# Kernel tuning notes

Measured on AMD Instinct MI355X. Metric: run time of the kernel, lower is better.

## Reference

```python
import jax, jax.numpy as jnp
import numpy as np

EPS = 1e-9
ALPHA = 1.0
BETA = 6.0
TOPK = 13
NUM_CLASSES = 80


def _make_boxes(key, shape, img=640.0, wh_min=8.0, wh_max=128.0):
    k1, k2 = jax.random.split(key)
    cxy = jax.random.uniform(k1, shape[:-1] + (2,)) * img
    wh = wh_min + jax.random.uniform(k2, shape[:-1] + (2,)) * (wh_max - wh_min)
    return jnp.concatenate([cxy - wh / 2, cxy + wh / 2], axis=-1)


def setup_inputs() -> dict:
    key = jax.random.key(0)
    ks = jax.random.split(key, 5)
    B, N, C, M = 16, 8400, NUM_CLASSES, 64
    pd_scores = jax.random.normal(ks[0], (B, N, C), dtype=jnp.float32)  # logits
    pd_bboxes = _make_boxes(ks[1], (B, N, 4))
    anc_points = jax.random.uniform(ks[2], (N, 2)) * 640.0
    gt_labels = jax.random.randint(ks[3], (B, M, 1), 0, C).astype(jnp.int64)
    gt_bboxes = _make_boxes(ks[4], (B, M, 4), wh_min=16.0, wh_max=256.0)
    mask_gt = jnp.ones((B, M, 1), dtype=jnp.float32)
    return {"pd_scores": pd_scores, "pd_bboxes": pd_bboxes, "anc_points": anc_points,
            "gt_labels": gt_labels, "gt_bboxes": gt_bboxes, "mask_gt": mask_gt}


def _pairwise_iou(gt_bboxes, pd_bboxes):
    # gt: (B,M,4), pd: (B,N,4) -> (B,M,N)
    a1 = gt_bboxes[:, :, None, :2]
    a2 = gt_bboxes[:, :, None, 2:]
    b1 = pd_bboxes[:, None, :, :2]
    b2 = pd_bboxes[:, None, :, 2:]
    inter = jnp.clip(jnp.minimum(a2, b2) - jnp.maximum(a1, b1), 0.0).prod(-1)
    area_a = (a2 - a1).prod(-1)
    area_b = (b2 - b1).prod(-1)
    return inter / jnp.maximum(area_a + area_b - inter, EPS)


def _tal_assign(pd_scores, pd_bboxes, anc_points, gt_labels, gt_bboxes, mask_gt):
    B, N, C = pd_scores.shape
    M = gt_labels.shape[1]
    ps = jax.nn.sigmoid(pd_scores)  # input_is_logits=True
    mask_gt_bool = mask_gt[..., 0] > 0.5  # (B,M)

    # centers-in-boxes mask (B,M,N)
    xy = anc_points[None, None, :, :]
    lt = gt_bboxes[:, :, None, :2]
    rb = gt_bboxes[:, :, None, 2:]
    deltas = jnp.concatenate([xy - lt, rb - xy], axis=-1)  # (B,M,N,4)
    mask_in_gts = deltas.min(-1) > EPS
    valid = mask_in_gts & mask_gt_bool[:, :, None]

    # alignment metric: score(gt class)^alpha * IoU^beta, zero outside valid
    gt_ids = jnp.clip(gt_labels[..., 0], 0)  # (B,M)
    scores_t = jnp.swapaxes(ps, 1, 2)  # (B,C,N)
    bbox_scores = jnp.take_along_axis(scores_t, gt_ids[:, :, None], axis=1)  # (B,M,N)
    ious = _pairwise_iou(gt_bboxes, pd_bboxes)
    ious = jnp.where(valid, ious, 0.0)
    align = jnp.where(valid, (bbox_scores ** ALPHA) * (ious ** BETA), 0.0)

    # top-k anchors per GT along anchor dim
    topv, topi = jax.lax.top_k(align, TOPK)  # (B,M,K)
    sel = (topv > EPS) & mask_gt_bool[:, :, None]
    bi = jnp.arange(B)[:, None, None]
    mi = jnp.arange(M)[None, :, None]
    cnt = jnp.zeros((B, M, N), jnp.int32).at[bi, mi, topi].add(sel.astype(jnp.int32))
    topk_mask = cnt > 0
    mask_pos = (topk_mask & valid).astype(jnp.float32)  # (B,M,N)

    # resolve anchors assigned to multiple GTs: keep highest IoU GT
    fg = mask_pos.sum(axis=1)  # (B,N)
    multi = (fg > 1)[:, None, :]  # (B,1,N)
    best_gt = jnp.argmax(ious, axis=1)  # (B,N)
    is_max = jnp.swapaxes(jax.nn.one_hot(best_gt, M, dtype=mask_pos.dtype), 1, 2)  # (B,M,N)
    mask_pos = jnp.where(multi, is_max, mask_pos)
    fg_mask = mask_pos.sum(axis=1)  # (B,N)
    tgt_gt_idx = jnp.argmax(mask_pos, axis=1)  # (B,N)

    # gather targets
    target_labels = jnp.take_along_axis(gt_labels[..., 0], tgt_gt_idx, axis=1)  # (B,N)
    target_bboxes = jnp.take_along_axis(gt_bboxes, tgt_gt_idx[..., None], axis=1)  # (B,N,4)

    # normalized classification targets
    align = align * mask_pos
    max_align = align.max(axis=1, keepdims=True) + EPS  # (B,1,N)
    per_anchor = (align / max_align * (ious * mask_pos)).sum(axis=1)  # (B,N)
    onehot = jax.nn.one_hot(target_labels, C, dtype=jnp.float32)
    cls_targets = onehot * per_anchor[..., None]  # (B,N,C)
    return target_labels, target_bboxes, cls_targets, fg_mask > 0, tgt_gt_idx


def reference(pd_scores, pd_bboxes, anc_points, gt_labels, gt_bboxes, mask_gt):
    return _tal_assign(pd_scores, pd_bboxes, anc_points, gt_labels, gt_bboxes, mask_gt)
```

## Files before the change

kernel.cpp:

```cpp
#include <hip/hip_runtime.h>
#include <math.h>

#define BB 16
#define NN 8400
#define CC 80
#define MM 64
#define KTOP 13
#define FEPS 1e-9f
#define CAP 2048
#define RPW 8

typedef float floatx4 __attribute__((ext_vector_type(4)));

#define OFF_O1 134400
#define OFF_O2 672000
#define OFF_O3 11424000
#define OFF_O4 11558400
#define CCNT_OFF 9299200
#define CAND_OFF 9300224
#define SCR_OFF  10348800

__device__ __forceinline__ float iou_pair(const float4 g, const float4 p) {
    float ix1 = fmaxf(g.x, p.x);
    float iy1 = fmaxf(g.y, p.y);
    float ix2 = fminf(g.z, p.z);
    float iy2 = fminf(g.w, p.w);
    float iw = fmaxf(ix2 - ix1, 0.0f);
    float ih = fmaxf(iy2 - iy1, 0.0f);
    float inter = iw * ih;
    float aa = (g.z - g.x) * (g.w - g.y);
    float ab = (p.z - p.x) * (p.w - p.y);
    float uni = fmaxf(aa + ab - inter, FEPS);
    return inter / uni;
}

__global__ __launch_bounds__(256) void k_zero2(int* __restrict__ ccnt,
                                               int* __restrict__ scr)
{
    int i = blockIdx.x * 256 + threadIdx.x;
    if (i < 1024) ccnt[i] = 0;
    else if (i < 1024 + 403200) scr[i - 1024] = 0;
}

__global__ __launch_bounds__(256) void k_inbox(
    const float* __restrict__ anc, const float* __restrict__ gt_bboxes,
    const float* __restrict__ mask_gt,
    int* __restrict__ ccnt, unsigned short* __restrict__ cand)
{
    const int b = blockIdx.y;
    const int n = blockIdx.x * 256 + threadIdx.x;
    const int tid = threadIdx.x;

    __shared__ float4 gtb[MM];
    __shared__ int hcnt[MM];
    __shared__ int gbase[MM];

    if (tid < MM) {
        float4 g = *(const float4*)&gt_bboxes[(size_t)(b * MM + tid) * 4];
        if (mask_gt[b * MM + tid] <= 0.5f)
            g = make_float4(1e30f, 1e30f, -1e30f, -1e30f);
        gtb[tid] = g;
        hcnt[tid] = 0;
    }
    __syncthreads();

    float ax = 0.0f, ay = 0.0f;
    const bool inb = n < NN;
    if (inb) { float2 a2 = *(const float2*)&anc[2 * n]; ax = a2.x; ay = a2.y; }

    unsigned long long mask = 0ull;
    #pragma unroll 8
    for (int m = 0; m < MM; ++m) {
        float4 g = gtb[m];
        float d1 = ax - g.x, d2 = ay - g.y, d3 = g.z - ax, d4 = g.w - ay;
        if (inb && fminf(fminf(d1, d2), fminf(d3, d4)) > FEPS)
            mask |= 1ull << m;
    }

    unsigned long long t = mask;
    while (t) { int m = __ffsll(t) - 1; t &= t - 1; atomicAdd(&hcnt[m], 1); }
    __syncthreads();

    if (tid < MM && hcnt[tid] > 0) {
        gbase[tid] = atomicAdd(&ccnt[b * MM + tid], hcnt[tid]);
        hcnt[tid] = 0;
    }
    __syncthreads();

    t = mask;
    while (t) {
        int m = __ffsll(t) - 1; t &= t - 1;
        int slot = gbase[m] + atomicAdd(&hcnt[m], 1);
        if (slot < CAP)
            cand[(size_t)(b * MM + m) * CAP + slot] = (unsigned short)n;
    }
}

__global__ __launch_bounds__(256) void k_topk(
    const float* __restrict__ pd_scores, const float* __restrict__ pd_bboxes,
    const int* __restrict__ gt_labels, const float* __restrict__ gt_bboxes,
    const int* __restrict__ ccnt, const unsigned short* __restrict__ cand,
    int* __restrict__ cntb, int* __restrict__ mselb, float* __restrict__ aselb)
{
    const int bm = blockIdx.x;
    const int b = bm >> 6, m = bm & 63;
    const int tid = threadIdx.x;
    const int lane = tid & 63;
    const int wid = tid >> 6;

    __shared__ unsigned long long cmerge[64];

    const float4 g = *(const float4*)&gt_bboxes[(size_t)bm * 4];
    const int lab  = gt_labels[bm];
    const int labc = lab > 0 ? lab : 0;
    const unsigned epskey = __float_as_uint(FEPS);
    const int count = min(ccnt[bm], CAP);
    const unsigned short* list = cand + (size_t)bm * CAP;
    const float* srow = pd_scores + (size_t)b * NN * CC + labc;
    const float* pbb  = pd_bboxes + (size_t)b * NN * 4;

    unsigned long long e[RPW];
    #pragma unroll
    for (int j = 0; j < RPW; ++j) {
        int i = tid + j * 256;
        unsigned long long v = 0ull;
        if (i < count) {
            int n = list[i];
            float4 p = *(const float4*)&pbb[(size_t)n * 4];
            float io = iou_pair(g, p);
            float x = srow[(size_t)n * CC];
            float s = 1.0f / (1.0f + expf(-x));
            float i2 = io * io;
            unsigned key = __float_as_uint(s * (i2 * i2 * i2));
            v = ((unsigned long long)key << 32) | (unsigned)(NN - n);
        }
        e[j] = v;
    }

    {
        unsigned long long lm = 0ull;
        #pragma unroll
        for (int j = 0; j < RPW; ++j) if (e[j] > lm) lm = e[j];

        unsigned long long winv = 0ull;
        for (int r = 0; r < KTOP; ++r) {
            unsigned long long bv = lm;
            #pragma unroll
            for (int off = 32; off > 0; off >>= 1) {
                unsigned long long ov = __shfl_xor(bv, off, 64);
                if (ov > bv) bv = ov;
            }
            if ((unsigned)(bv >> 32) <= epskey) break;
            if (lane == r) winv = bv;
            if (lm == bv) {
                #pragma unroll
                for (int j = 0; j < RPW; ++j) if (e[j] == bv) e[j] = 0ull;
                lm = 0ull;
                #pragma unroll
                for (int j = 0; j < RPW; ++j) if (e[j] > lm) lm = e[j];
            }
        }
        if (lane < KTOP) cmerge[wid * KTOP + lane] = winv;
        if (wid == 0 && lane >= 4 * KTOP) cmerge[lane] = 0ull;
    }
    __syncthreads();

    if (wid == 0) {
        unsigned long long v = cmerge[lane];
        unsigned long long winv = 0ull;
        for (int r = 0; r < KTOP; ++r) {
            unsigned long long bv = v;
            #pragma unroll
            for (int off = 32; off > 0; off >>= 1) {
                unsigned long long ov = __shfl_xor(bv, off, 64);
                if (ov > bv) bv = ov;
            }
            if ((unsigned)(bv >> 32) <= epskey) break;
            if (lane == r) winv = bv;
            if (v == bv) v = 0ull;
        }
        if (lane < KTOP) {
            unsigned hk = (unsigned)(winv >> 32);
            if (hk > epskey) {
                int n = NN - (int)(winv & 0xFFFFFFFFull);
                int ai = b * NN + n;
                atomicAdd(&cntb[ai], 1);
                atomicAdd(&mselb[ai], m);
                atomicAdd(&aselb[ai], __uint_as_float(hk));
            }
        }
    }
}

__global__ __launch_bounds__(256) void k_assign(
    const float* __restrict__ pd_scores, const float* __restrict__ pd_bboxes,
    const float* __restrict__ anc, const int* __restrict__ gt_labels,
    const float* __restrict__ gt_bboxes, const float* __restrict__ mask_gt,
    const int* __restrict__ cntb, const int* __restrict__ mselb,
    const float* __restrict__ aselb,
    float* __restrict__ out0, float* __restrict__ out1,
    float* __restrict__ out3, float* __restrict__ out4,
    float* __restrict__ perb)
{
    const int b = blockIdx.y;
    const int n = blockIdx.x * 256 + threadIdx.x;

    __shared__ float4 gtb[MM];
    __shared__ int    labS[MM];
    __shared__ float  mgS[MM];
    if (threadIdx.x < MM) {
        int m = threadIdx.x;
        gtb[m]  = *(const float4*)&gt_bboxes[(size_t)(b * MM + m) * 4];
        labS[m] = gt_labels[b * MM + m];
        mgS[m]  = mask_gt[b * MM + m];
    }
    __syncthreads();
    if (n >= NN) return;

    const size_t idx = (size_t)b * NN + n;
    const int cnt = cntb[idx];

    float per = 0.0f, fg = 0.0f;
    int mstar = 0;

    if (cnt > 0) {
        fg = 1.0f;
        const float4 p = *(const float4*)&pd_bboxes[idx * 4];
        if (cnt == 1) {
            mstar = mselb[idx];
            float a = aselb[idx];
            float io = iou_pair(gtb[mstar], p);
            per = a / (a + FEPS) * io;
        } else {
            float2 a2 = *(const float2*)&anc[2 * n];
            float bestI = -1.0f; int bestM = 0;
            for (int m = 0; m < MM; ++m) {
                float4 gg = gtb[m];
                float d1 = a2.x - gg.x, d2 = a2.y - gg.y;
                float d3 = gg.z - a2.x, d4 = gg.w - a2.y;
                bool valid = (fminf(fminf(d1, d2), fminf(d3, d4)) > FEPS) &&
                             (mgS[m] > 0.5f);
                float io = valid ? iou_pair(gg, p) : 0.0f;
                if (io > bestI) { bestI = io; bestM = m; }
            }
            mstar = bestM;
            float io = bestI;
            int lb = labS[mstar]; int lbc = lb > 0 ? lb : 0;
            float x = pd_scores[idx * CC + lbc];
            float s = 1.0f / (1.0f + expf(-x));
            float i2 = io * io;
            float a = s * (i2 * i2 * i2);
            per = a / (a + FEPS) * io;
        }
    }

    out0[idx] = (float)labS[mstar];
    ((float4*)out1)[idx] = gtb[mstar];
    out3[idx] = fg;
    out4[idx] = (float)mstar;
    perb[idx] = per;
}

__global__ __launch_bounds__(256) void k_cls(
    const float* __restrict__ out0, const float* __restrict__ perb,
    floatx4* __restrict__ cls4)
{
    int i = blockIdx.x * 256 + threadIdx.x;
    if (i >= BB * NN * CC / 4) return;
    int row = i / 20;
    int c4 = (i - row * 20) * 4;
    int lab = (int)out0[row];
    float per = perb[row];
    int d = lab - c4;
    floatx4 v;
    v.x = (d == 0) ? per : 0.0f;
    v.y = (d == 1) ? per : 0.0f;
    v.z = (d == 2) ? per : 0.0f;
    v.w = (d == 3) ? per : 0.0f;
    __builtin_nontemporal_store(v, &cls4[i]);
}

extern "C" void kernel_launch(void* const* d_in, const int* in_sizes, int n_in,
                              void* d_out, int out_size, void* d_ws, size_t ws_size,
                              hipStream_t stream) {
    const float* pd_scores = (const float*)d_in[0];
    const float* pd_bboxes = (const float*)d_in[1];
    const float* anc       = (const float*)d_in[2];
    const int*   gt_labels = (const int*)d_in[3];
    const float* gt_bboxes = (const float*)d_in[4];
    const float* mask_gt   = (const float*)d_in[5];

    float* out  = (float*)d_out;
    float* out0 = out;
    float* out1 = out + OFF_O1;
    float* out2 = out + OFF_O2;
    float* out3 = out + OFF_O3;
    float* out4 = out + OFF_O4;

    int*            ccnt  = (int*)(out2 + CCNT_OFF);
    unsigned short* cand  = (unsigned short*)(out2 + CAND_OFF);
    float*          scr   = out2 + SCR_OFF;
    int*            cntb  = (int*)scr;
    int*            mselb = (int*)(scr + 134400);
    float*          aselb = scr + 268800;
    float*          perb  = (float*)d_ws;

    k_zero2<<<dim3((1024 + 403200 + 255) / 256), dim3(256), 0, stream>>>(
        ccnt, (int*)scr);

    k_inbox<<<dim3((NN + 255) / 256, BB), dim3(256), 0, stream>>>(
        anc, gt_bboxes, mask_gt, ccnt, cand);

    k_topk<<<dim3(BB * MM), dim3(256), 0, stream>>>(
        pd_scores, pd_bboxes, gt_labels, gt_bboxes, ccnt, cand,
        cntb, mselb, aselb);

    k_assign<<<dim3((NN + 255) / 256, BB), dim3(256), 0, stream>>>(
        pd_scores, pd_bboxes, anc, gt_labels, gt_bboxes, mask_gt,
        cntb, mselb, aselb, out0, out1, out3, out4, perb);

    const int n4 = (BB * NN * CC) / 4;
    k_cls<<<dim3((n4 + 255) / 256), dim3(256), 0, stream>>>(out0, perb, (floatx4*)out2);
}
```

Measured before the change: 64.65 us.

## Compute alignment keys in the in-box pass and emit packed candidates

Moves the IoU, sigmoid and alignment-metric computation from the per-GT top-k kernel into the per-anchor in-box kernel. Each candidate slot now holds a packed 64-bit key/index, so top-k only loads precomputed keys. This replaces scattered gathers of scores and boxes per GT with anchor-local reads of a row that covers all of that anchor's GTs. In exchange the candidate buffer grows from 16-bit to 64-bit entries, and the scratch offsets are moved to fit it.

```diff
diff --git a/kernel.cpp b/kernel.cpp
--- a/kernel.cpp
+++ b/kernel.cpp
@@ -11,13 +11,14 @@
 #define RPW 8
 
 typedef float floatx4 __attribute__((ext_vector_type(4)));
+typedef unsigned long long u64;
 
 #define OFF_O1 134400
 #define OFF_O2 672000
 #define OFF_O3 11424000
 #define OFF_O4 11558400
-#define CCNT_OFF 9299200
-#define CAND_OFF 9300224
+#define CCNT_OFF 6153472
+#define CAND_OFF 6154496
 #define SCR_OFF  10348800
 
 __device__ __forceinline__ float iou_pair(const float4 g, const float4 p) {
@@ -42,16 +43,18 @@
     else if (i < 1024 + 403200) scr[i - 1024] = 0;
 }
 
-__global__ __launch_bounds__(256) void k_inbox(
-    const float* __restrict__ anc, const float* __restrict__ gt_bboxes,
-    const float* __restrict__ mask_gt,
-    int* __restrict__ ccnt, unsigned short* __restrict__ cand)
+__global__ __launch_bounds__(256) void k_align_emit(
+    const float* __restrict__ pd_scores, const float* __restrict__ pd_bboxes,
+    const float* __restrict__ anc, const int* __restrict__ gt_labels,
+    const float* __restrict__ gt_bboxes, const float* __restrict__ mask_gt,
+    int* __restrict__ ccnt, u64* __restrict__ cand)
 {
     const int b = blockIdx.y;
     const int n = blockIdx.x * 256 + threadIdx.x;
     const int tid = threadIdx.x;
 
     __shared__ float4 gtb[MM];
+    __shared__ int labS[MM];
     __shared__ int hcnt[MM];
     __shared__ int gbase[MM];
 
@@ -60,6 +63,8 @@
         if (mask_gt[b * MM + tid] <= 0.5f)
             g = make_float4(1e30f, 1e30f, -1e30f, -1e30f);
         gtb[tid] = g;
+        int lb = gt_labels[b * MM + tid];
+        labS[tid] = lb > 0 ? lb : 0;
         hcnt[tid] = 0;
     }
     __syncthreads();
@@ -68,7 +73,7 @@
     const bool inb = n < NN;
     if (inb) { float2 a2 = *(const float2*)&anc[2 * n]; ax = a2.x; ay = a2.y; }
 
-    unsigned long long mask = 0ull;
+    u64 mask = 0ull;
     #pragma unroll 8
     for (int m = 0; m < MM; ++m) {
         float4 g = gtb[m];
@@ -77,29 +82,39 @@
             mask |= 1ull << m;
     }
 
-    unsigned long long t = mask;
+    u64 t = mask;
     while (t) { int m = __ffsll(t) - 1; t &= t - 1; atomicAdd(&hcnt[m], 1); }
     __syncthreads();
-
     if (tid < MM && hcnt[tid] > 0) {
         gbase[tid] = atomicAdd(&ccnt[b * MM + tid], hcnt[tid]);
         hcnt[tid] = 0;
     }
     __syncthreads();
 
-    t = mask;
-    while (t) {
-        int m = __ffsll(t) - 1; t &= t - 1;
-        int slot = gbase[m] + atomicAdd(&hcnt[m], 1);
-        if (slot < CAP)
-            cand[(size_t)(b * MM + m) * CAP + slot] = (unsigned short)n;
+    if (mask) {
+        const float4 p = *(const float4*)&pd_bboxes[((size_t)b * NN + n) * 4];
+        const float* srow = pd_scores + ((size_t)b * NN + n) * CC;
+        t = mask;
+        while (t) {
+            int m = __ffsll(t) - 1; t &= t - 1;
+            float io = iou_pair(gtb[m], p);
+            int lab = labS[m];
+            float4 c = *(const float4*)(srow + (lab & ~3));
+            int r = lab & 3;
+            float x = (r == 0) ? c.x : (r == 1) ? c.y : (r == 2) ? c.z : c.w;
+            float s = 1.0f / (1.0f + expf(-x));
+            float i2 = io * io;
+            unsigned key = __float_as_uint(s * (i2 * i2 * i2));
+            int slot = gbase[m] + atomicAdd(&hcnt[m], 1);
+            if (slot < CAP)
+                cand[(size_t)(b * MM + m) * CAP + slot] =
+                    ((u64)key << 32) | (unsigned)(NN - n);
+        }
     }
 }
 
 __global__ __launch_bounds__(256) void k_topk(
-    const float* __restrict__ pd_scores, const float* __restrict__ pd_bboxes,
-    const int* __restrict__ gt_labels, const float* __restrict__ gt_bboxes,
-    const int* __restrict__ ccnt, const unsigned short* __restrict__ cand,
+    const int* __restrict__ ccnt, const u64* __restrict__ cand,
     int* __restrict__ cntb, int* __restrict__ mselb, float* __restrict__ aselb)
 {
     const int bm = blockIdx.x;
@@ -108,46 +123,30 @@
     const int lane = tid & 63;
     const int wid = tid >> 6;
 
-    __shared__ unsigned long long cmerge[64];
-
-    const float4 g = *(const float4*)&gt_bboxes[(size_t)bm * 4];
-    const int lab  = gt_labels[bm];
-    const int labc = lab > 0 ? lab : 0;
+    __shared__ u64 cmerge[64];
+
     const unsigned epskey = __float_as_uint(FEPS);
     const int count = min(ccnt[bm], CAP);
-    const unsigned short* list = cand + (size_t)bm * CAP;
-    const float* srow = pd_scores + (size_t)b * NN * CC + labc;
-    const float* pbb  = pd_bboxes + (size_t)b * NN * 4;
-
-    unsigned long long e[RPW];
+    const u64* list = cand + (size_t)bm * CAP;
+
+    u64 e[RPW];
     #pragma unroll
     for (int j = 0; j < RPW; ++j) {
         int i = tid + j * 256;
-        unsigned long long v = 0ull;
-        if (i < count) {
-            int n = list[i];
-            float4 p = *(const float4*)&pbb[(size_t)n * 4];
-            float io = iou_pair(g, p);
-            float x = srow[(size_t)n * CC];
-            float s = 1.0f / (1.0f + expf(-x));
-            float i2 = io * io;
-            unsigned key = __float_as_uint(s * (i2 * i2 * i2));
-            v = ((unsigned long long)key << 32) | (unsigned)(NN - n);
-        }
-        e[j] = v;
+        e[j] = (i < count) ? list[i] : 0ull;
     }
 
     {
-        unsigned long long lm = 0ull;
+        u64 lm = 0ull;
         #pragma unroll
         for (int j = 0; j < RPW; ++j) if (e[j] > lm) lm = e[j];
 
-        unsigned long long winv = 0ull;
+        u64 winv = 0ull;
         for (int r = 0; r < KTOP; ++r) {
-            unsigned long long bv = lm;
+            u64 bv = lm;
             #pragma unroll
             for (int off = 32; off > 0; off >>= 1) {
-                unsigned long long ov = __shfl_xor(bv, off, 64);
+                u64 ov = __shfl_xor(bv, off, 64);
                 if (ov > bv) bv = ov;
             }
             if ((unsigned)(bv >> 32) <= epskey) break;
@@ -166,13 +165,13 @@
     __syncthreads();
 
     if (wid == 0) {
-        unsigned long long v = cmerge[lane];
-        unsigned long long winv = 0ull;
+        u64 v = cmerge[lane];
+        u64 winv = 0ull;
         for (int r = 0; r < KTOP; ++r) {
-            unsigned long long bv = v;
+            u64 bv = v;
             #pragma unroll
             for (int off = 32; off > 0; off >>= 1) {
-                unsigned long long ov = __shfl_xor(bv, off, 64);
+                u64 ov = __shfl_xor(bv, off, 64);
                 if (ov > bv) bv = ov;
             }
             if ((unsigned)(bv >> 32) <= epskey) break;
@@ -297,23 +296,22 @@
     float* out3 = out + OFF_O3;
     float* out4 = out + OFF_O4;
 
-    int*            ccnt  = (int*)(out2 + CCNT_OFF);
-    unsigned short* cand  = (unsigned short*)(out2 + CAND_OFF);
-    float*          scr   = out2 + SCR_OFF;
-    int*            cntb  = (int*)scr;
-    int*            mselb = (int*)(scr + 134400);
-    float*          aselb = scr + 268800;
-    float*          perb  = (float*)d_ws;
+    int*   ccnt  = (int*)(out2 + CCNT_OFF);
+    u64*   cand  = (u64*)(out2 + CAND_OFF);
+    float* scr   = out2 + SCR_OFF;
+    int*   cntb  = (int*)scr;
+    int*   mselb = (int*)(scr + 134400);
+    float* aselb = scr + 268800;
+    float* perb  = (float*)d_ws;
 
     k_zero2<<<dim3((1024 + 403200 + 255) / 256), dim3(256), 0, stream>>>(
         ccnt, (int*)scr);
 
-    k_inbox<<<dim3((NN + 255) / 256, BB), dim3(256), 0, stream>>>(
-        anc, gt_bboxes, mask_gt, ccnt, cand);
+    k_align_emit<<<dim3((NN + 255) / 256, BB), dim3(256), 0, stream>>>(
+        pd_scores, pd_bboxes, anc, gt_labels, gt_bboxes, mask_gt, ccnt, cand);
 
     k_topk<<<dim3(BB * MM), dim3(256), 0, stream>>>(
-        pd_scores, pd_bboxes, gt_labels, gt_bboxes, ccnt, cand,
-        cntb, mselb, aselb);
+        ccnt, cand, cntb, mselb, aselb);
 
     k_assign<<<dim3((NN + 255) / 256, BB), dim3(256), 0, stream>>>(
         pd_scores, pd_bboxes, anc, gt_labels, gt_bboxes, mask_gt,
```

New measurement: 64.15 us. About the same (-0.8%).
